# Performance work log

Measured on AMD Instinct MI355X. Metric: run time of the kernel, lower is better.

Reference implementation:

```python
import jax, jax.numpy as jnp
import numpy as np

N_VOXELS = 1024
N_RAYS = 2048
SH_DEGREE = 2
N_SH = 9            # (sh_degree+1)^2 with degree-2 real SH basis (1+3+5 terms)
S = 8               # ray_samples_per_voxel
BG_COLOR = (0.0, 0.0, 0.0)
FAR_PLANE = 100.0
EARLY_STOP_T = 0.01 # transmittance early-termination threshold from the torch loop


def eval_sh_basis(degree, dirs):
    # dirs: [..., 3] -> [..., N_SH]
    x, y, z = dirs[..., 0], dirs[..., 1], dirs[..., 2]
    sh = [jnp.ones_like(x)]
    if degree >= 1:
        sh += [y, z, x]
    if degree >= 2:
        sh += [x * y, y * z, 3 * z ** 2 - 1, x * z, x ** 2 - y ** 2]
    if degree >= 3:
        sh += [y * (3 * x ** 2 - y ** 2), x * y * z, y * (5 * z ** 2 - 1),
               z * (5 * z ** 2 - 3), x * (5 * z ** 2 - 1), (x ** 2 - y ** 2) * z,
               x * (x ** 2 - 3 * y ** 2)]
    return jnp.stack(sh, axis=-1)


def setup_inputs() -> dict:
    key = jax.random.key(0)
    ks = jax.random.split(key, 6)
    positions = jax.random.uniform(ks[0], (N_VOXELS, 3), minval=-1.0, maxval=1.0)
    sizes = 0.05 + 0.15 * jax.random.uniform(ks[1], (N_VOXELS,))
    densities = jax.random.normal(ks[2], (N_VOXELS,))
    colors = 0.3 * jax.random.normal(ks[3], (N_VOXELS, 3 * N_SH))
    ray_origins = jnp.array([0.0, 0.0, -3.0]) + 0.1 * jax.random.normal(ks[4], (N_RAYS, 3))
    targets = jax.random.uniform(ks[5], (N_RAYS, 3), minval=-1.0, maxval=1.0)
    d = targets - ray_origins
    ray_directions = d / jnp.linalg.norm(d, axis=-1, keepdims=True)
    return {"positions": positions, "sizes": sizes, "densities": densities,
            "colors": colors, "ray_origins": ray_origins, "ray_directions": ray_directions}


def _forward(positions, sizes, densities, colors, ray_o, ray_d):
    B = ray_o.shape[0]
    N = positions.shape[0]
    # ---- AABB intersection for all (ray, voxel) pairs ----
    half = (sizes / 2.0)[:, None]                      # [N,1]
    bmin = positions - half                            # [N,3]
    bmax = positions + half
    inv_d = 1.0 / ray_d                                # [B,3]
    t0 = (bmin[None, :, :] - ray_o[:, None, :]) * inv_d[:, None, :]   # [B,N,3]
    t1 = (bmax[None, :, :] - ray_o[:, None, :]) * inv_d[:, None, :]
    t_near = jnp.max(jnp.minimum(t0, t1), axis=-1)     # [B,N]
    t_far = jnp.min(jnp.maximum(t0, t1), axis=-1)
    valid = (t_far > t_near) & (t_far > 0.0)
    # sanitize invalid entries so no inf/nan leaks into masked-out math
    tn = jnp.where(valid, t_near, 0.0)
    tf = jnp.where(valid, t_far, 1.0)

    # ---- per-ray SH color (rgb_samples is constant across samples: dirs = ray_d) ----
    sh = eval_sh_basis(SH_DEGREE, ray_d)               # [B,C]
    coeffs = colors.reshape(N, 3, N_SH)                # [N,3,C]
    rgb_vox = jax.nn.sigmoid(jnp.einsum('bc,nkc->bnk', sh, coeffs))   # [B,N,3]

    # ---- within-voxel alpha compositing (S samples, constant sigma per voxel) ----
    sigma = jnp.exp(densities)                         # [N], density_activation='exp'
    delta = (tf - tn) / S                              # [B,N]
    alpha = 1.0 - jnp.exp(-sigma[None, :] * delta)     # [B,N]
    base = 1.0 - alpha + 1e-8
    i = jnp.arange(S, dtype=jnp.float32)
    pw = base[..., None] ** i                          # [B,N,S] exclusive cumprod of (1-a)
    w = alpha[..., None] * pw                          # per-sample weights
    frac = i / (S - 1)                                 # linspace(t_near, t_far, S)
    t_s = tn[..., None] + (tf - tn)[..., None] * frac  # [B,N,S]
    ws = jnp.where(valid, jnp.sum(w, -1), 0.0)         # [B,N] weight_sum per voxel
    depth_vox = jnp.where(valid, jnp.sum(w * t_s, -1), 0.0)

    # ---- sort voxels per ray by entry distance (invalid -> end) ----
    key_t = jnp.where(valid, tn, jnp.inf)
    order = jnp.argsort(key_t, axis=-1)                # [B,N]
    ws_s = jnp.take_along_axis(ws, order, -1)
    dep_s = jnp.take_along_axis(depth_vox, order, -1)
    rgb_s = jnp.take_along_axis(rgb_vox, order[..., None], 1)

    # ---- sequential compositing across voxels (closed form, with early-stop mask) ----
    one_m = 1.0 - ws_s
    T_before = jnp.cumprod(
        jnp.concatenate([jnp.ones((B, 1), one_m.dtype), one_m[:, :-1]], -1), axis=-1)
    proc = (T_before >= EARLY_STOP_T).astype(one_m.dtype)  # voxels processed before break
    contrib = T_before * ws_s * proc                   # [B,N]
    rgb_acc = jnp.einsum('bn,bnk->bk', contrib, rgb_s) # [B,3]
    depth_acc = jnp.sum(T_before * proc * dep_s, -1)   # [B]
    weight_acc = jnp.sum(contrib, -1)                  # [B]
    T_final = jnp.prod(1.0 - ws_s * proc, -1)          # transmittance at break/end

    bg = jnp.asarray(BG_COLOR, dtype=rgb_acc.dtype)
    rgb_acc = rgb_acc + T_final[:, None] * bg
    has_hit = valid.any(-1)
    depth = jnp.where(has_hit, depth_acc, FAR_PLANE)[:, None]
    return rgb_acc, depth, weight_acc[:, None]


def reference(positions, sizes, densities, colors, ray_origins, ray_directions):
    return _forward(positions, sizes, densities, colors, ray_origins, ray_directions)
```

## Files before the change

### kernel.cpp

```cpp
#include <hip/hip_runtime.h>

#define NMAX 1024
#define BLOCK 256

__global__ __launch_bounds__(BLOCK) void voxel_raster_kernel(
    const float* __restrict__ positions, const float* __restrict__ sizes,
    const float* __restrict__ densities, const float* __restrict__ colors,
    const float* __restrict__ ray_o, const float* __restrict__ ray_d,
    float* __restrict__ out, int N, int B)
{
    const int b   = blockIdx.x;
    const int tid = threadIdx.x;

    __shared__ int cnt;
    __shared__ unsigned long long skey[NMAX];
    __shared__ float sws[NMAX], sdep[NMAX];
    __shared__ float sr[NMAX], sg[NMAX], sb[NMAX];

    if (tid == 0) cnt = 0;
    __syncthreads();

    const float ox = ray_o[b * 3 + 0], oy = ray_o[b * 3 + 1], oz = ray_o[b * 3 + 2];
    const float dx = ray_d[b * 3 + 0], dy = ray_d[b * 3 + 1], dz = ray_d[b * 3 + 2];
    const float ivx = 1.0f / dx, ivy = 1.0f / dy, ivz = 1.0f / dz;

    float sh[9];
    sh[0] = 1.0f;  sh[1] = dy;      sh[2] = dz;           sh[3] = dx;
    sh[4] = dx*dy; sh[5] = dy*dz;   sh[6] = 3.0f*dz*dz-1.0f;
    sh[7] = dx*dz; sh[8] = dx*dx - dy*dy;

    for (int n = tid; n < N; n += BLOCK) {
        const float half = sizes[n] * 0.5f;
        const float px = positions[n * 3 + 0];
        const float py = positions[n * 3 + 1];
        const float pz = positions[n * 3 + 2];

        float t0 = (px - half - ox) * ivx, t1 = (px + half - ox) * ivx;
        float tn = fminf(t0, t1), tf = fmaxf(t0, t1);
        t0 = (py - half - oy) * ivy; t1 = (py + half - oy) * ivy;
        tn = fmaxf(tn, fminf(t0, t1)); tf = fminf(tf, fmaxf(t0, t1));
        t0 = (pz - half - oz) * ivz; t1 = (pz + half - oz) * ivz;
        tn = fmaxf(tn, fminf(t0, t1)); tf = fminf(tf, fmaxf(t0, t1));

        const bool valid = (tf > tn) && (tf > 0.0f);
        if (!valid) continue;

        const float sigma = expf(densities[n]);
        const float dt    = tf - tn;
        const float alpha = 1.0f - expf(-sigma * dt * 0.125f);
        const float base  = 1.0f - alpha + 1e-8f;
        float pw = 1.0f, ws = 0.0f, dep = 0.0f;
        #pragma unroll
        for (int i = 0; i < 8; i++) {
            const float w  = alpha * pw;
            const float ts = tn + dt * ((float)i * (1.0f / 7.0f));
            ws  += w;
            dep += w * ts;
            pw  *= base;
        }

        float rgb[3];
        #pragma unroll
        for (int k = 0; k < 3; k++) {
            float acc = 0.0f;
            #pragma unroll
            for (int c = 0; c < 9; c++)
                acc += sh[c] * colors[n * 27 + k * 9 + c];
            rgb[k] = 1.0f / (1.0f + expf(-acc));
        }

        const int slot = atomicAdd(&cnt, 1);
        unsigned u = __float_as_uint(tn);
        u = (u & 0x80000000u) ? ~u : (u | 0x80000000u);
        skey[slot] = ((unsigned long long)u << 32) |
                     ((unsigned long long)(unsigned)n << 16) |
                     (unsigned long long)(unsigned)slot;
        sws[slot]  = ws;
        sdep[slot] = dep;
        sr[slot] = rgb[0]; sg[slot] = rgb[1]; sb[slot] = rgb[2];
    }
    __syncthreads();

    const int m = cnt;
    int P = 1;
    while (P < m) P <<= 1;
    for (int i = m + tid; i < P; i += BLOCK)
        skey[i] = 0xFFFFFFFFFFFFFFFFull;

    if (m > 1) {
        for (int k = 2; k <= P; k <<= 1) {
            for (int j = k >> 1; j > 0; j >>= 1) {
                __syncthreads();
                for (int i = tid; i < P; i += BLOCK) {
                    const int ixj = i ^ j;
                    if (ixj > i) {
                        const unsigned long long a = skey[i];
                        const unsigned long long c = skey[ixj];
                        const bool up = ((i & k) == 0);
                        if ((a > c) == up) { skey[i] = c; skey[ixj] = a; }
                    }
                }
            }
        }
    }
    __syncthreads();

    if (tid == 0) {
        float T = 1.0f, ra = 0.f, ga = 0.f, ba = 0.f, da = 0.f, wa = 0.f;
        for (int i = 0; i < m; i++) {
            if (T < 0.01f) break;
            const int slot = (int)(skey[i] & 0xFFFFull);
            const float w  = sws[slot];
            const float cw = T * w;
            ra += cw * sr[slot];
            ga += cw * sg[slot];
            ba += cw * sb[slot];
            da += T * sdep[slot];
            wa += cw;
            T *= (1.0f - w);
        }
        out[b * 3 + 0] = ra;
        out[b * 3 + 1] = ga;
        out[b * 3 + 2] = ba;
        out[B * 3 + b] = (m > 0) ? da : 100.0f;
        out[B * 4 + b] = wa;
    }
}

extern "C" void kernel_launch(void* const* d_in, const int* in_sizes, int n_in,
                              void* d_out, int out_size, void* d_ws, size_t ws_size,
                              hipStream_t stream) {
    const float* positions = (const float*)d_in[0];
    const float* sizes     = (const float*)d_in[1];
    const float* densities = (const float*)d_in[2];
    const float* colors    = (const float*)d_in[3];
    const float* ray_o     = (const float*)d_in[4];
    const float* ray_d     = (const float*)d_in[5];
    const int N = in_sizes[1];
    const int B = in_sizes[4] / 3;

    voxel_raster_kernel<<<B, BLOCK, 0, stream>>>(
        positions, sizes, densities, colors, ray_o, ray_d,
        (float*)d_out, N, B);
}
```

Baseline: 76.37 us.

## Replace per-ray block sort with wave-level incremental min-selection compositing

Each ray now maps to one 64-lane wavefront instead of a full 256-thread block. The wave computes entry distances for all voxels in registers, then repeatedly picks the nearest remaining hit with a wave-wide shuffle min-reduction and composites it, stopping once transmittance falls below the threshold. This removes the shared-memory bitonic sort, the atomics and the many block barriers, and only shades voxels that are actually composited. The cost is a serial loop whose length equals the number of composited voxels, with only one lane doing useful shading per step. N is hardcoded to 1024 through CH=16.

```diff
diff --git a/kernel.cpp b/kernel.cpp
--- a/kernel.cpp
+++ b/kernel.cpp
@@ -1,49 +1,94 @@
 #include <hip/hip_runtime.h>
 
-#define NMAX 1024
-#define BLOCK 256
 
-__global__ __launch_bounds__(BLOCK) void voxel_raster_kernel(
+#define CH 16
+#define EARLY_STOP 0.01f
+
+__device__ __forceinline__ unsigned long long shfl_xor_u64(unsigned long long v, int m) {
+    unsigned lo = (unsigned)v, hi = (unsigned)(v >> 32);
+    lo = __shfl_xor(lo, m, 64);
+    hi = __shfl_xor(hi, m, 64);
+    return ((unsigned long long)hi << 32) | lo;
+}
+
+__global__ __launch_bounds__(256) void voxel_raster_wave(
     const float* __restrict__ positions, const float* __restrict__ sizes,
     const float* __restrict__ densities, const float* __restrict__ colors,
     const float* __restrict__ ray_o, const float* __restrict__ ray_d,
-    float* __restrict__ out, int N, int B)
+    float* __restrict__ out, int B)
 {
-    const int b   = blockIdx.x;
-    const int tid = threadIdx.x;
+    const int lane = threadIdx.x & 63;
+    const int r    = blockIdx.x * 4 + (threadIdx.x >> 6);
+    if (r >= B) return;
 
-    __shared__ int cnt;
-    __shared__ unsigned long long skey[NMAX];
-    __shared__ float sws[NMAX], sdep[NMAX];
-    __shared__ float sr[NMAX], sg[NMAX], sb[NMAX];
-
-    if (tid == 0) cnt = 0;
-    __syncthreads();
-
-    const float ox = ray_o[b * 3 + 0], oy = ray_o[b * 3 + 1], oz = ray_o[b * 3 + 2];
-    const float dx = ray_d[b * 3 + 0], dy = ray_d[b * 3 + 1], dz = ray_d[b * 3 + 2];
+    const float ox = ray_o[r * 3 + 0], oy = ray_o[r * 3 + 1], oz = ray_o[r * 3 + 2];
+    const float dx = ray_d[r * 3 + 0], dy = ray_d[r * 3 + 1], dz = ray_d[r * 3 + 2];
     const float ivx = 1.0f / dx, ivy = 1.0f / dy, ivz = 1.0f / dz;
 
     float sh[9];
-    sh[0] = 1.0f;  sh[1] = dy;      sh[2] = dz;           sh[3] = dx;
-    sh[4] = dx*dy; sh[5] = dy*dz;   sh[6] = 3.0f*dz*dz-1.0f;
+    sh[0] = 1.0f;  sh[1] = dy;    sh[2] = dz;              sh[3] = dx;
+    sh[4] = dx*dy; sh[5] = dy*dz; sh[6] = 3.0f*dz*dz-1.0f;
     sh[7] = dx*dz; sh[8] = dx*dx - dy*dy;
 
-    for (int n = tid; n < N; n += BLOCK) {
+    float tnr[CH];
+    unsigned vmask = 0;
+    #pragma unroll
+    for (int c = 0; c < CH; ++c) {
+        const int n = c * 64 + lane;
         const float half = sizes[n] * 0.5f;
         const float px = positions[n * 3 + 0];
         const float py = positions[n * 3 + 1];
         const float pz = positions[n * 3 + 2];
+        float a0 = (px - half - ox) * ivx, a1 = (px + half - ox) * ivx;
+        float tn = fminf(a0, a1), tf = fmaxf(a0, a1);
+        a0 = (py - half - oy) * ivy; a1 = (py + half - oy) * ivy;
+        tn = fmaxf(tn, fminf(a0, a1)); tf = fminf(tf, fmaxf(a0, a1));
+        a0 = (pz - half - oz) * ivz; a1 = (pz + half - oz) * ivz;
+        tn = fmaxf(tn, fminf(a0, a1)); tf = fminf(tf, fmaxf(a0, a1));
+        tnr[c] = tn;
+        if ((tf > tn) && (tf > 0.0f)) vmask |= (1u << c);
+    }
 
-        float t0 = (px - half - ox) * ivx, t1 = (px + half - ox) * ivx;
-        float tn = fminf(t0, t1), tf = fmaxf(t0, t1);
-        t0 = (py - half - oy) * ivy; t1 = (py + half - oy) * ivy;
-        tn = fmaxf(tn, fminf(t0, t1)); tf = fminf(tf, fmaxf(t0, t1));
-        t0 = (pz - half - oz) * ivz; t1 = (pz + half - oz) * ivz;
-        tn = fmaxf(tn, fminf(t0, t1)); tf = fminf(tf, fmaxf(t0, t1));
+    const bool has_hit = __any(vmask != 0);
 
-        const bool valid = (tf > tn) && (tf > 0.0f);
-        if (!valid) continue;
+    float T = 1.0f, ra = 0.f, ga = 0.f, ba = 0.f, da = 0.f, wa = 0.f;
+    for (;;) {
+        unsigned long long best = ~0ull;
+        #pragma unroll
+        for (int c = 0; c < CH; ++c) {
+            if (vmask & (1u << c)) {
+                unsigned u = __float_as_uint(tnr[c]);
+                u = (u & 0x80000000u) ? ~u : (u | 0x80000000u);
+                const unsigned long long k =
+                    ((unsigned long long)u << 32) | (unsigned)(c * 64 + lane);
+                if (k < best) best = k;
+            }
+        }
+        #pragma unroll
+        for (int off = 32; off > 0; off >>= 1) {
+            const unsigned long long o = shfl_xor_u64(best, off);
+            if (o < best) best = o;
+        }
+        if (best == ~0ull) break;
+        if (T < EARLY_STOP) break;
+
+        const int n = (int)(best & 0xFFFFFFFFu);
+        if (lane == (n & 63)) vmask &= ~(1u << (n >> 6));
+
+        unsigned u = (unsigned)(best >> 32);
+        u = (u & 0x80000000u) ? (u ^ 0x80000000u) : ~u;
+        const float tn = __uint_as_float(u);
+
+        const float half = sizes[n] * 0.5f;
+        const float px = positions[n * 3 + 0];
+        const float py = positions[n * 3 + 1];
+        const float pz = positions[n * 3 + 2];
+        float a0 = (px - half - ox) * ivx, a1 = (px + half - ox) * ivx;
+        float tf = fmaxf(a0, a1);
+        a0 = (py - half - oy) * ivy; a1 = (py + half - oy) * ivy;
+        tf = fminf(tf, fmaxf(a0, a1));
+        a0 = (pz - half - oz) * ivz; a1 = (pz + half - oz) * ivz;
+        tf = fminf(tf, fmaxf(a0, a1));
 
         const float sigma = expf(densities[n]);
         const float dt    = tf - tn;
@@ -69,61 +114,21 @@
             rgb[k] = 1.0f / (1.0f + expf(-acc));
         }
 
-        const int slot = atomicAdd(&cnt, 1);
-        unsigned u = __float_as_uint(tn);
-        u = (u & 0x80000000u) ? ~u : (u | 0x80000000u);
-        skey[slot] = ((unsigned long long)u << 32) |
-                     ((unsigned long long)(unsigned)n << 16) |
-                     (unsigned long long)(unsigned)slot;
-        sws[slot]  = ws;
-        sdep[slot] = dep;
-        sr[slot] = rgb[0]; sg[slot] = rgb[1]; sb[slot] = rgb[2];
+        const float cw = T * ws;
+        ra += cw * rgb[0];
+        ga += cw * rgb[1];
+        ba += cw * rgb[2];
+        da += T * dep;
+        wa += cw;
+        T  *= (1.0f - ws);
     }
-    __syncthreads();
 
-    const int m = cnt;
-    int P = 1;
-    while (P < m) P <<= 1;
-    for (int i = m + tid; i < P; i += BLOCK)
-        skey[i] = 0xFFFFFFFFFFFFFFFFull;
-
-    if (m > 1) {
-        for (int k = 2; k <= P; k <<= 1) {
-            for (int j = k >> 1; j > 0; j >>= 1) {
-                __syncthreads();
-                for (int i = tid; i < P; i += BLOCK) {
-                    const int ixj = i ^ j;
-                    if (ixj > i) {
-                        const unsigned long long a = skey[i];
-                        const unsigned long long c = skey[ixj];
-                        const bool up = ((i & k) == 0);
-                        if ((a > c) == up) { skey[i] = c; skey[ixj] = a; }
-                    }
-                }
-            }
-        }
-    }
-    __syncthreads();
-
-    if (tid == 0) {
-        float T = 1.0f, ra = 0.f, ga = 0.f, ba = 0.f, da = 0.f, wa = 0.f;
-        for (int i = 0; i < m; i++) {
-            if (T < 0.01f) break;
-            const int slot = (int)(skey[i] & 0xFFFFull);
-            const float w  = sws[slot];
-            const float cw = T * w;
-            ra += cw * sr[slot];
-            ga += cw * sg[slot];
-            ba += cw * sb[slot];
-            da += T * sdep[slot];
-            wa += cw;
-            T *= (1.0f - w);
-        }
-        out[b * 3 + 0] = ra;
-        out[b * 3 + 1] = ga;
-        out[b * 3 + 2] = ba;
-        out[B * 3 + b] = (m > 0) ? da : 100.0f;
-        out[B * 4 + b] = wa;
+    if (lane == 0) {
+        out[r * 3 + 0] = ra;
+        out[r * 3 + 1] = ga;
+        out[r * 3 + 2] = ba;
+        out[B * 3 + r] = has_hit ? da : 100.0f;
+        out[B * 4 + r] = wa;
     }
 }
 
@@ -136,10 +141,8 @@
     const float* colors    = (const float*)d_in[3];
     const float* ray_o     = (const float*)d_in[4];
     const float* ray_d     = (const float*)d_in[5];
-    const int N = in_sizes[1];
     const int B = in_sizes[4] / 3;
 
-    voxel_raster_kernel<<<B, BLOCK, 0, stream>>>(
-        positions, sizes, densities, colors, ray_o, ray_d,
-        (float*)d_out, N, B);
+    voxel_raster_wave<<<(B + 3) / 4, 256, 0, stream>>>(
+        positions, sizes, densities, colors, ray_o, ray_d, (float*)d_out, B);
 }
```

After: 84.05 us. 1.1x slower.
